# Kernel tuning notes

Measured on AMD Instinct MI355X. Metric: run time of the kernel, lower is better.

The kernel has to match this reference:

```python
import jax, jax.numpy as jnp
import numpy as np

NEG = 1e9  # mask value added to already-selected positions (original uses -1e9)


def setup_inputs() -> dict:
    key = jax.random.key(0)
    ks = jax.random.split(key, 12)
    B, N, M = 8, 2048, 256
    s = 0.05  # keep gates/softmax in a sane range
    return dict(
        node_embedding=jax.random.normal(ks[0], (B, N, M), dtype=jnp.float32),
        z_g=jax.random.normal(ks[1], (B, M), dtype=jnp.float32) * s,
        decoder_init=jax.random.normal(ks[2], (M,), dtype=jnp.float32) * s,
        hidden0=jax.random.normal(ks[3], (M,), dtype=jnp.float32) * s,
        w_ih=jax.random.normal(ks[4], (4 * M, M), dtype=jnp.float32) * s,
        w_hh=jax.random.normal(ks[5], (4 * M, M), dtype=jnp.float32) * s,
        b_ih=jax.random.normal(ks[6], (4 * M,), dtype=jnp.float32) * s,
        b_hh=jax.random.normal(ks[7], (4 * M,), dtype=jnp.float32) * s,
        Wq=jax.random.normal(ks[8], (M, M), dtype=jnp.float32) * s,
        bq=jax.random.normal(ks[9], (M,), dtype=jnp.float32) * s,
        Wk=jax.random.normal(ks[10], (M, M), dtype=jnp.float32) * s,
        bk=jax.random.normal(ks[11], (M,), dtype=jnp.float32) * s,
    )


def reference(node_embedding, z_g, decoder_init, hidden0,
              w_ih, w_hh, b_ih, b_hh, Wq, bq, Wk, bk):
    # Returns the per-step masked softmax attention distributions [B, N, N]
    # (row t = distribution over boxes at decode step t; argmax of each row
    #  is the predicted order, and selected indices are masked out).
    N = node_embedding.shape[1]
    # LSTM input is the constant decoder_init every step -> precompute its proj.
    x_proj = decoder_init @ w_ih.T + b_ih  # [4M]

    def decode_one(z_g_b, node_emb_b):
        keys = node_emb_b @ Wk.T + bk  # [N, M] (self.key(node_embedding))

        def step(carry, _):
            h, c, used = carry
            # torch LSTMCell: gates ordered (i, f, g, o)
            gates = x_proj + h @ w_hh.T + b_hh  # [4M]
            i_g, f_g, g_g, o_g = jnp.split(gates, 4)
            i_g = jax.nn.sigmoid(i_g)
            f_g = jax.nn.sigmoid(f_g)
            g_g = jnp.tanh(g_g)
            o_g = jax.nn.sigmoid(o_g)
            c = f_g * c + i_g * g_g
            h = o_g * jnp.tanh(c)
            q = h @ Wq.T + bq                    # [M]
            scores = keys @ q                    # [N]
            scores = jnp.where(used, scores - NEG, scores)  # mask selected
            probs = jax.nn.softmax(scores)       # [N]
            idx = jnp.argmax(probs)              # top-1 pointer selection
            used = used.at[idx].set(True)
            return (h, c, used), probs

        init = (hidden0, z_g_b, jnp.zeros((N,), dtype=bool))
        _, probs = jax.lax.scan(step, init, None, length=N)
        return probs  # [N, N]

    return jax.vmap(decode_one)(z_g, node_embedding)  # [B, N, N]
```

## Files before the change

### kernel.cpp

```cpp
#include <hip/hip_runtime.h>
#include <cstdint>
#include <cstddef>

#define NB 8
#define NN 2048
#define MM 256

typedef unsigned long long u64;

__device__ __forceinline__ unsigned mapf(float f) {
  unsigned u = __float_as_uint(f + 0.f);
  return ((int)u >= 0) ? (u ^ 0x80000000u) : ~u;
}
__device__ __forceinline__ u64 shflx_u64(u64 v, int m) {
  unsigned lo = (unsigned)__shfl_xor((int)(unsigned)v, m);
  unsigned hi = (unsigned)__shfl_xor((int)(v >> 32), m);
  return ((u64)hi << 32) | lo;
}

__global__ __launch_bounds__(1024) void lstm_kernel(
    const float* __restrict__ z_g, const float* __restrict__ dec,
    const float* __restrict__ h0, const float* __restrict__ w_ih,
    const float* __restrict__ w_hh, const float* __restrict__ b_ih,
    const float* __restrict__ b_hh, float* __restrict__ Hall,
    u64* __restrict__ Pbuf)
{
  const int b = blockIdx.x;
  const int q = blockIdx.y;
  const int tid = threadIdx.x;
  const int w = tid >> 6;
  const int lane = tid & 63;
  const int rr = lane >> 3;
  const int c8 = lane & 7;
  const int lr = 8 * w + rr;
  const int g = lr >> 5;
  const int m = lr & 31;
  const int grow = g * 256 + 32 * q + m;

  __shared__ __align__(16) float hbuf[256];
  __shared__ __align__(16) float act[128];

  float wreg[32];
  {
    const float* wr = w_hh + (size_t)grow * MM + 32 * c8;
    #pragma unroll
    for (int jj = 0; jj < 8; ++jj) {
      float4 v = *(const float4*)(wr + 4 * ((jj + c8) & 7));
      wreg[4 * jj + 0] = v.x; wreg[4 * jj + 1] = v.y;
      wreg[4 * jj + 2] = v.z; wreg[4 * jj + 3] = v.w;
    }
  }

  float xb;
  {
    const float* wr = w_ih + (size_t)grow * MM + 32 * c8;
    float p = 0.f;
    #pragma unroll
    for (int i = 0; i < 8; ++i) {
      float4 wv = *(const float4*)(wr + 4 * i);
      float4 dv = *(const float4*)(dec + 32 * c8 + 4 * i);
      p += wv.x * dv.x + wv.y * dv.y + wv.z * dv.z + wv.w * dv.w;
    }
    p += __shfl_xor(p, 1); p += __shfl_xor(p, 2); p += __shfl_xor(p, 4);
    xb = p + b_ih[grow] + b_hh[grow];
  }

  float c_my = 0.f;
  if (tid < 32) c_my = z_g[b * MM + 32 * q + tid];
  if (tid < 256) hbuf[tid] = h0[tid];

  u64* Pb = Pbuf + (size_t)b * 512;
  float* Hb = Hall + (size_t)b * NN * MM + 32 * q;

  for (int tt = 0; tt < NN; ++tt) {
    if (tt > 0 && w < 4) {
      const int widx = (w << 6) + lane;
      const u64* pa = Pb + ((tt & 1) << 8) + widx;
      u64 v = __hip_atomic_load(pa, __ATOMIC_RELAXED,
                                __HIP_MEMORY_SCOPE_AGENT);
      bool ok = ((unsigned)(v >> 32) == (unsigned)tt);
      while (!__all((int)ok)) {
        if (!ok) {
          v = __hip_atomic_load(pa, __ATOMIC_RELAXED,
                                __HIP_MEMORY_SCOPE_AGENT);
          ok = ((unsigned)(v >> 32) == (unsigned)tt);
        }
      }
      hbuf[widx] = __uint_as_float((unsigned)v);
    }
    __syncthreads();

    float a0 = 0.f, a1 = 0.f, a2 = 0.f, a3 = 0.f;
    const float4* h4 = (const float4*)hbuf;
    #pragma unroll
    for (int jj = 0; jj < 8; ++jj) {
      float4 hv = h4[8 * c8 + ((jj + c8) & 7)];
      a0 = fmaf(hv.x, wreg[4 * jj + 0], a0);
      a1 = fmaf(hv.y, wreg[4 * jj + 1], a1);
      a2 = fmaf(hv.z, wreg[4 * jj + 2], a2);
      a3 = fmaf(hv.w, wreg[4 * jj + 3], a3);
    }
    float s = (a0 + a1) + (a2 + a3);
    s += __shfl_xor(s, 1); s += __shfl_xor(s, 2); s += __shfl_xor(s, 4);
    const float gsum = s + xb;

    float a;
    if ((w >> 2) == 2) { const float e = __expf(-2.f * gsum); a = 2.f / (1.f + e) - 1.f; }
    else               { a = 1.f / (1.f + __expf(-gsum)); }
    if (c8 == 0) act[lr] = a;
    __syncthreads();

    if (tid < 32) {
      const float i_g = act[tid], f_g = act[32 + tid];
      const float g_g = act[64 + tid], o_g = act[96 + tid];
      c_my = f_g * c_my + i_g * g_g;
      const float e2 = __expf(-2.f * c_my);
      const float hn = o_g * (2.f / (1.f + e2) - 1.f);
      const u64 pk = ((u64)(unsigned)(tt + 1) << 32) | (u64)__float_as_uint(hn);
      __hip_atomic_store(Pb + (((tt + 1) & 1) << 8) + 32 * q + tid, pk,
                         __ATOMIC_RELAXED, __HIP_MEMORY_SCOPE_AGENT);
      Hb[(size_t)tt * MM + tid] = hn;
    }
  }
}

__global__ __launch_bounds__(256) void gemm128(
    const float* __restrict__ A, const float* __restrict__ B,
    float* __restrict__ C, const float* __restrict__ bias,
    int K, int Ncol, long sA, long sB, long sC)
{
  __shared__ __align__(16) float As[32][132];
  __shared__ __align__(16) float Bs[32][132];
  const int tid = threadIdx.x;
  const int tx = tid & 15;
  const int ty = tid >> 4;
  const int row0 = blockIdx.y * 128;
  const int col0 = blockIdx.x * 128;
  const float* Ab = A + (size_t)blockIdx.z * (size_t)sA;
  const float* Bb = B + (size_t)blockIdx.z * (size_t)sB;
  float* Cb = C + (size_t)blockIdx.z * (size_t)sC;

  float acc[8][8];
  #pragma unroll
  for (int i = 0; i < 8; ++i)
    #pragma unroll
    for (int jj = 0; jj < 8; ++jj) acc[i][jj] = 0.f;

  for (int k0 = 0; k0 < K; k0 += 32) {
    #pragma unroll
    for (int it = 0; it < 4; ++it) {
      const int idx = tid + it * 256;
      const int r = idx >> 3;
      const int c4 = (idx & 7) << 2;
      float4 va = *(const float4*)(Ab + (size_t)(row0 + r) * K + k0 + c4);
      float4 vb = *(const float4*)(Bb + (size_t)(col0 + r) * K + k0 + c4);
      As[c4 + 0][r] = va.x; As[c4 + 1][r] = va.y;
      As[c4 + 2][r] = va.z; As[c4 + 3][r] = va.w;
      Bs[c4 + 0][r] = vb.x; Bs[c4 + 1][r] = vb.y;
      Bs[c4 + 2][r] = vb.z; Bs[c4 + 3][r] = vb.w;
    }
    __syncthreads();
    #pragma unroll
    for (int kk = 0; kk < 32; ++kk) {
      float4 a0 = *(const float4*)&As[kk][ty * 4];
      float4 a1 = *(const float4*)&As[kk][64 + ty * 4];
      float4 b0 = *(const float4*)&Bs[kk][tx * 4];
      float4 b1 = *(const float4*)&Bs[kk][64 + tx * 4];
      const float av[8] = {a0.x, a0.y, a0.z, a0.w, a1.x, a1.y, a1.z, a1.w};
      const float bv[8] = {b0.x, b0.y, b0.z, b0.w, b1.x, b1.y, b1.z, b1.w};
      #pragma unroll
      for (int i = 0; i < 8; ++i)
        #pragma unroll
        for (int jj = 0; jj < 8; ++jj)
          acc[i][jj] = fmaf(av[i], bv[jj], acc[i][jj]);
    }
    __syncthreads();
  }

  #pragma unroll
  for (int i = 0; i < 8; ++i) {
    const int r = row0 + ((i < 4) ? (ty * 4 + i) : (64 + ty * 4 + i - 4));
    float* cp = Cb + (size_t)r * Ncol + col0;
    float4 o0, o1;
    float* o0p = &o0.x; float* o1p = &o1.x;
    #pragma unroll
    for (int jj = 0; jj < 4; ++jj) {
      float v0 = acc[i][jj], v1 = acc[i][jj + 4];
      if (bias) {
        v0 += bias[col0 + tx * 4 + jj];
        v1 += bias[col0 + 64 + tx * 4 + jj];
      }
      o0p[jj] = v0; o1p[jj] = v1;
    }
    *(float4*)(cp + tx * 4) = o0;
    *(float4*)(cp + 64 + tx * 4) = o1;
  }
}

__global__ __launch_bounds__(512) void select_block(
    const float* __restrict__ S, int* __restrict__ sel)
{
  const int b = blockIdx.x;
  const int tid = threadIdx.x;
  const int w = tid >> 6;
  const int lane = tid & 63;
  const float* Sb = S + (size_t)b * NN * NN + 4 * tid;
  int* selb = sel + b * NN;

  __shared__ u64 partial[2][8];

  for (int i = tid; i < NN; i += 512) selb[i] = 0x7fffffff;
  __syncthreads();

  unsigned mybits = 0;
  const unsigned base = 2047u - 4u * (unsigned)tid;

  auto stepf = [&](float4 v, int t) {
    u64 k0 = (mybits & 1u) ? 0 : (((u64)mapf(v.x) << 32) | (base - 0u));
    u64 k1 = (mybits & 2u) ? 0 : (((u64)mapf(v.y) << 32) | (base - 1u));
    u64 k2 = (mybits & 4u) ? 0 : (((u64)mapf(v.z) << 32) | (base - 2u));
    u64 k3 = (mybits & 8u) ? 0 : (((u64)mapf(v.w) << 32) | (base - 3u));
    u64 k = k0 > k1 ? k0 : k1;
    if (k2 > k) k = k2;
    if (k3 > k) k = k3;
    #pragma unroll
    for (int off = 1; off < 64; off <<= 1) {
      u64 o = shflx_u64(k, off);
      if (o > k) k = o;
    }
    if (lane == 0) partial[t & 1][w] = k;
    __syncthreads();
    u64 pk = partial[t & 1][lane & 7];
    #pragma unroll
    for (int off = 1; off < 8; off <<= 1) {
      u64 o = shflx_u64(pk, off);
      if (o > pk) pk = o;
    }
    const int idx = 2047 - (int)(pk & 0x7ff);
    if ((idx >> 2) == tid) mybits |= 1u << (idx & 3);
    if (tid == 0) selb[idx] = t;
  };

  float4 r0 = *(const float4*)(Sb + (size_t)0 * NN);
  float4 r1 = *(const float4*)(Sb + (size_t)1 * NN);
  float4 r2 = *(const float4*)(Sb + (size_t)2 * NN);
  float4 r3 = *(const float4*)(Sb + (size_t)3 * NN);
  for (int t = 0; t < NN; t += 4) {
    const size_t p4 = (size_t)((t + 4 < NN) ? t + 4 : NN - 1) * NN;
    const size_t p5 = (size_t)((t + 5 < NN) ? t + 5 : NN - 1) * NN;
    const size_t p6 = (size_t)((t + 6 < NN) ? t + 6 : NN - 1) * NN;
    const size_t p7 = (size_t)((t + 7 < NN) ? t + 7 : NN - 1) * NN;
    stepf(r0, t);     r0 = *(const float4*)(Sb + p4);
    stepf(r1, t + 1); r1 = *(const float4*)(Sb + p5);
    stepf(r2, t + 2); r2 = *(const float4*)(Sb + p6);
    stepf(r3, t + 3); r3 = *(const float4*)(Sb + p7);
  }
}

__global__ __launch_bounds__(256) void softmax_kernel(
    float* __restrict__ out, const int* __restrict__ sel)
{
  const int t = blockIdx.x;
  const int b = blockIdx.y;
  const int tid = threadIdx.x;
  float* row = out + ((size_t)b * NN + t) * NN;
  const int* selb = sel + b * NN;
  __shared__ float red[8];

  float v[8];
  int sl[8];
  #pragma unroll
  for (int u = 0; u < 2; ++u) {
    float4 f = *(const float4*)(row + u * 1024 + tid * 4);
    int4 s4 = *(const int4*)(selb + u * 1024 + tid * 4);
    v[u * 4 + 0] = f.x; v[u * 4 + 1] = f.y; v[u * 4 + 2] = f.z; v[u * 4 + 3] = f.w;
    sl[u * 4 + 0] = s4.x; sl[u * 4 + 1] = s4.y; sl[u * 4 + 2] = s4.z; sl[u * 4 + 3] = s4.w;
  }

  float mx = -3.0e38f;
  #pragma unroll
  for (int e = 0; e < 8; ++e)
    if (sl[e] >= t) mx = fmaxf(mx, v[e]);
  #pragma unroll
  for (int off = 1; off < 64; off <<= 1) mx = fmaxf(mx, __shfl_xor(mx, off));
  if ((tid & 63) == 0) red[tid >> 6] = mx;
  __syncthreads();
  mx = fmaxf(fmaxf(red[0], red[1]), fmaxf(red[2], red[3]));

  float e8[8];
  float sum = 0.f;
  #pragma unroll
  for (int e = 0; e < 8; ++e) {
    float ex = (sl[e] >= t) ? __expf(v[e] - mx) : 0.f;
    e8[e] = ex;
    sum += ex;
  }
  #pragma unroll
  for (int off = 1; off < 64; off <<= 1) sum += __shfl_xor(sum, off);
  if ((tid & 63) == 0) red[4 + (tid >> 6)] = sum;
  __syncthreads();
  sum = red[4] + red[5] + red[6] + red[7];
  const float inv = 1.f / sum;

  #pragma unroll
  for (int u = 0; u < 2; ++u) {
    float4 o;
    o.x = e8[u * 4 + 0] * inv; o.y = e8[u * 4 + 1] * inv;
    o.z = e8[u * 4 + 2] * inv; o.w = e8[u * 4 + 3] * inv;
    *(float4*)(row + u * 1024 + tid * 4) = o;
  }
}

extern "C" void kernel_launch(void* const* d_in, const int* in_sizes, int n_in,
                              void* d_out, int out_size, void* d_ws, size_t ws_size,
                              hipStream_t stream)
{
  (void)in_sizes; (void)n_in; (void)out_size; (void)ws_size;
  const float* emb  = (const float*)d_in[0];
  const float* z_g  = (const float*)d_in[1];
  const float* dec  = (const float*)d_in[2];
  const float* h0   = (const float*)d_in[3];
  const float* w_ih = (const float*)d_in[4];
  const float* w_hh = (const float*)d_in[5];
  const float* b_ih = (const float*)d_in[6];
  const float* b_hh = (const float*)d_in[7];
  const float* Wq   = (const float*)d_in[8];
  const float* bq   = (const float*)d_in[9];
  const float* Wk   = (const float*)d_in[10];
  const float* bk   = (const float*)d_in[11];
  float* out = (float*)d_out;
  float* ws  = (float*)d_ws;

  float* keys  = ws;
  float* Q     = ws + 4194304;
  u64*   Pbuf  = (u64*)(ws + 8388608);
  int*   sel   = (int*)(ws + 8396800);
  float* Hall  = out;

  hipMemsetAsync(Pbuf, 0, 4096 * sizeof(u64), stream);

  lstm_kernel<<<dim3(NB, 8), 1024, 0, stream>>>(
      z_g, dec, h0, w_ih, w_hh, b_ih, b_hh, Hall, Pbuf);

  gemm128<<<dim3(MM / 128, (NB * NN) / 128, 1), 256, 0, stream>>>(
      Hall, Wq, Q, bq, MM, MM, 0, 0, 0);

  gemm128<<<dim3(MM / 128, (NB * NN) / 128, 1), 256, 0, stream>>>(
      emb, Wk, keys, bk, MM, MM, 0, 0, 0);

  gemm128<<<dim3(NN / 128, NN / 128, NB), 256, 0, stream>>>(
      Q, keys, out, nullptr, MM, NN,
      (long)NN * MM, (long)NN * MM, (long)NN * NN);

  select_block<<<NB, 512, 0, stream>>>(out, sel);

  softmax_kernel<<<dim3(NN, NB), 256, 0, stream>>>(out, sel);
}
```

Measured before the change: 4.808 ms.

## Halve LSTM block size, keep gates per wave, drop second barrier

The LSTM recurrence kernel now runs 512 threads per block, and each thread computes two gate rows held in registers. The gate layout is arranged so that all four gates for a hidden unit sit in the same wavefront. Cell and hidden updates are therefore gathered with cross-lane shuffles instead of through shared memory. This removes one __syncthreads per step, and a double-buffered hbuf avoids a write-after-read race. The cost is more registers per thread, and the serial chain per step now runs two dot products in each thread.

```diff
diff --git a/kernel.cpp b/kernel.cpp
--- a/kernel.cpp
+++ b/kernel.cpp
@@ -18,7 +18,7 @@
   return ((u64)hi << 32) | lo;
 }
 
-__global__ __launch_bounds__(1024) void lstm_kernel(
+__global__ __launch_bounds__(512) void lstm_kernel(
     const float* __restrict__ z_g, const float* __restrict__ dec,
     const float* __restrict__ h0, const float* __restrict__ w_ih,
     const float* __restrict__ w_hh, const float* __restrict__ b_ih,
@@ -30,47 +30,59 @@
   const int tid = threadIdx.x;
   const int w = tid >> 6;
   const int lane = tid & 63;
-  const int rr = lane >> 3;
+  const int r8 = lane >> 3;
   const int c8 = lane & 7;
-  const int lr = 8 * w + rr;
-  const int g = lr >> 5;
-  const int m = lr & 31;
-  const int grow = g * 256 + 32 * q + m;
-
-  __shared__ __align__(16) float hbuf[256];
-  __shared__ __align__(16) float act[128];
-
-  float wreg[32];
+  const int g = r8 >> 1;
+  const int ml_lo = 4 * w + (r8 & 1);
+  const int grow_lo = g * 256 + 32 * q + ml_lo;
+  const int grow_hi = grow_lo + 2;
+  const int ml_own = r8 & 3;
+
+  __shared__ __align__(16) float hbuf[2][256];
+
+  float wlo[32], whi[32];
   {
-    const float* wr = w_hh + (size_t)grow * MM + 32 * c8;
+    const float* wr0 = w_hh + (size_t)grow_lo * MM + 32 * c8;
+    const float* wr1 = w_hh + (size_t)grow_hi * MM + 32 * c8;
     #pragma unroll
     for (int jj = 0; jj < 8; ++jj) {
-      float4 v = *(const float4*)(wr + 4 * ((jj + c8) & 7));
-      wreg[4 * jj + 0] = v.x; wreg[4 * jj + 1] = v.y;
-      wreg[4 * jj + 2] = v.z; wreg[4 * jj + 3] = v.w;
-    }
-  }
-
-  float xb;
+      const int sl = 4 * ((jj + c8) & 7);
+      float4 v = *(const float4*)(wr0 + sl);
+      wlo[4 * jj + 0] = v.x; wlo[4 * jj + 1] = v.y;
+      wlo[4 * jj + 2] = v.z; wlo[4 * jj + 3] = v.w;
+      float4 u = *(const float4*)(wr1 + sl);
+      whi[4 * jj + 0] = u.x; whi[4 * jj + 1] = u.y;
+      whi[4 * jj + 2] = u.z; whi[4 * jj + 3] = u.w;
+    }
+  }
+
+  float xb_lo, xb_hi;
   {
-    const float* wr = w_ih + (size_t)grow * MM + 32 * c8;
-    float p = 0.f;
+    const float* wr0 = w_ih + (size_t)grow_lo * MM + 32 * c8;
+    const float* wr1 = w_ih + (size_t)grow_hi * MM + 32 * c8;
+    float p0 = 0.f, p1 = 0.f;
     #pragma unroll
     for (int i = 0; i < 8; ++i) {
-      float4 wv = *(const float4*)(wr + 4 * i);
       float4 dv = *(const float4*)(dec + 32 * c8 + 4 * i);
-      p += wv.x * dv.x + wv.y * dv.y + wv.z * dv.z + wv.w * dv.w;
-    }
-    p += __shfl_xor(p, 1); p += __shfl_xor(p, 2); p += __shfl_xor(p, 4);
-    xb = p + b_ih[grow] + b_hh[grow];
-  }
-
-  float c_my = 0.f;
-  if (tid < 32) c_my = z_g[b * MM + 32 * q + tid];
-  if (tid < 256) hbuf[tid] = h0[tid];
+      float4 a = *(const float4*)(wr0 + 4 * i);
+      float4 c = *(const float4*)(wr1 + 4 * i);
+      p0 += a.x * dv.x + a.y * dv.y + a.z * dv.z + a.w * dv.w;
+      p1 += c.x * dv.x + c.y * dv.y + c.z * dv.z + c.w * dv.w;
+    }
+    p0 += __shfl_xor(p0, 1); p0 += __shfl_xor(p0, 2); p0 += __shfl_xor(p0, 4);
+    p1 += __shfl_xor(p1, 1); p1 += __shfl_xor(p1, 2); p1 += __shfl_xor(p1, 4);
+    xb_lo = p0 + b_ih[grow_lo] + b_hh[grow_lo];
+    xb_hi = p1 + b_ih[grow_hi] + b_hh[grow_hi];
+  }
+
+  float c_my = z_g[b * MM + 32 * q + 4 * w + ml_own];
+  if (tid < 256) hbuf[0][tid] = h0[tid];
 
   u64* Pb = Pbuf + (size_t)b * 512;
-  float* Hb = Hall + (size_t)b * NN * MM + 32 * q;
+  float* Hb = Hall + (size_t)b * NN * MM;
+
+  const bool istanh = (g == 2);
+  const float kmul = istanh ? -2.f : -1.f;
 
   for (int tt = 0; tt < NN; ++tt) {
     if (tt > 0 && w < 4) {
@@ -86,40 +98,63 @@
           ok = ((unsigned)(v >> 32) == (unsigned)tt);
         }
       }
-      hbuf[widx] = __uint_as_float((unsigned)v);
+      hbuf[tt & 1][widx] = __uint_as_float((unsigned)v);
     }
     __syncthreads();
 
-    float a0 = 0.f, a1 = 0.f, a2 = 0.f, a3 = 0.f;
-    const float4* h4 = (const float4*)hbuf;
+    const float4* h4 = (const float4*)hbuf[tt & 1];
+    float l0 = 0.f, l1 = 0.f, l2 = 0.f, l3 = 0.f;
+    float m0 = 0.f, m1 = 0.f, m2 = 0.f, m3 = 0.f;
     #pragma unroll
     for (int jj = 0; jj < 8; ++jj) {
       float4 hv = h4[8 * c8 + ((jj + c8) & 7)];
-      a0 = fmaf(hv.x, wreg[4 * jj + 0], a0);
-      a1 = fmaf(hv.y, wreg[4 * jj + 1], a1);
-      a2 = fmaf(hv.z, wreg[4 * jj + 2], a2);
-      a3 = fmaf(hv.w, wreg[4 * jj + 3], a3);
-    }
-    float s = (a0 + a1) + (a2 + a3);
-    s += __shfl_xor(s, 1); s += __shfl_xor(s, 2); s += __shfl_xor(s, 4);
-    const float gsum = s + xb;
-
-    float a;
-    if ((w >> 2) == 2) { const float e = __expf(-2.f * gsum); a = 2.f / (1.f + e) - 1.f; }
-    else               { a = 1.f / (1.f + __expf(-gsum)); }
-    if (c8 == 0) act[lr] = a;
-    __syncthreads();
-
-    if (tid < 32) {
-      const float i_g = act[tid], f_g = act[32 + tid];
-      const float g_g = act[64 + tid], o_g = act[96 + tid];
-      c_my = f_g * c_my + i_g * g_g;
-      const float e2 = __expf(-2.f * c_my);
-      const float hn = o_g * (2.f / (1.f + e2) - 1.f);
+      l0 = fmaf(hv.x, wlo[4 * jj + 0], l0);
+      l1 = fmaf(hv.y, wlo[4 * jj + 1], l1);
+      l2 = fmaf(hv.z, wlo[4 * jj + 2], l2);
+      l3 = fmaf(hv.w, wlo[4 * jj + 3], l3);
+      m0 = fmaf(hv.x, whi[4 * jj + 0], m0);
+      m1 = fmaf(hv.y, whi[4 * jj + 1], m1);
+      m2 = fmaf(hv.z, whi[4 * jj + 2], m2);
+      m3 = fmaf(hv.w, whi[4 * jj + 3], m3);
+    }
+    float s_lo = (l0 + l1) + (l2 + l3);
+    float s_hi = (m0 + m1) + (m2 + m3);
+    s_lo += __shfl_xor(s_lo, 1); s_lo += __shfl_xor(s_lo, 2); s_lo += __shfl_xor(s_lo, 4);
+    s_hi += __shfl_xor(s_hi, 1); s_hi += __shfl_xor(s_hi, 2); s_hi += __shfl_xor(s_hi, 4);
+    const float g_lo = s_lo + xb_lo;
+    const float g_hi = s_hi + xb_hi;
+
+    float e = __expf(kmul * g_lo);
+    float sg = 1.f / (1.f + e);
+    const float a_lo = istanh ? 2.f * sg - 1.f : sg;
+    e = __expf(kmul * g_hi);
+    sg = 1.f / (1.f + e);
+    const float a_hi = istanh ? 2.f * sg - 1.f : sg;
+
+    const int baseLane = 8 * (r8 & 1) + c8;
+    const bool lohalf = (r8 & 2) == 0;
+    float gi, gf, gg_, go;
+    {
+      float tl = __shfl(a_lo, baseLane);      float th = __shfl(a_hi, baseLane);
+      gi = lohalf ? tl : th;
+      tl = __shfl(a_lo, baseLane + 16);       th = __shfl(a_hi, baseLane + 16);
+      gf = lohalf ? tl : th;
+      tl = __shfl(a_lo, baseLane + 32);       th = __shfl(a_hi, baseLane + 32);
+      gg_ = lohalf ? tl : th;
+      tl = __shfl(a_lo, baseLane + 48);       th = __shfl(a_hi, baseLane + 48);
+      go = lohalf ? tl : th;
+    }
+
+    c_my = gf * c_my + gi * gg_;
+    const float e2 = __expf(-2.f * c_my);
+    const float hn = go * (2.f / (1.f + e2) - 1.f);
+
+    if (c8 == 0 && r8 < 4) {
+      const int mi = 32 * q + 4 * w + r8;
       const u64 pk = ((u64)(unsigned)(tt + 1) << 32) | (u64)__float_as_uint(hn);
-      __hip_atomic_store(Pb + (((tt + 1) & 1) << 8) + 32 * q + tid, pk,
+      __hip_atomic_store(Pb + (((tt + 1) & 1) << 8) + mi, pk,
                          __ATOMIC_RELAXED, __HIP_MEMORY_SCOPE_AGENT);
-      Hb[(size_t)tt * MM + tid] = hn;
+      Hb[(size_t)tt * MM + mi] = hn;
     }
   }
 }
@@ -339,7 +374,7 @@
 
   hipMemsetAsync(Pbuf, 0, 4096 * sizeof(u64), stream);
 
-  lstm_kernel<<<dim3(NB, 8), 1024, 0, stream>>>(
+  lstm_kernel<<<dim3(NB, 8), 512, 0, stream>>>(
       z_g, dec, h0, w_ih, w_hh, b_ih, b_hh, Hall, Pbuf);
 
   gemm128<<<dim3(MM / 128, (NB * NN) / 128, 1), 256, 0, stream>>>(
```

Result: slower. 6.637 ms (+38.0%).

## Remap LSTM gate rows per wave to drop second barrier and use shuffles

Applied to the files above, without the earlier changes.

Reassigns hidden units so each wave holds all four gate rows (i,f,g,o) for two hidden units. The gate activations can then be combined with wave shuffles instead of a shared-memory act buffer and a second __syncthreads per step. The h buffer is double-buffered so the single barrier per step is enough, and the spin-wait on the cross-block h exchange keeps three outstanding loads in flight to cut polling latency. The cost is extra polling traffic and redundant cell-state updates across lanes.

```diff
diff --git a/kernel.cpp b/kernel.cpp
--- a/kernel.cpp
+++ b/kernel.cpp
@@ -16,6 +16,9 @@
   unsigned lo = (unsigned)__shfl_xor((int)(unsigned)v, m);
   unsigned hi = (unsigned)__shfl_xor((int)(v >> 32), m);
   return ((u64)hi << 32) | lo;
+}
+__device__ __forceinline__ u64 agent_load(const u64* p) {
+  return __hip_atomic_load(p, __ATOMIC_RELAXED, __HIP_MEMORY_SCOPE_AGENT);
 }
 
 __global__ __launch_bounds__(1024) void lstm_kernel(
@@ -30,15 +33,14 @@
   const int tid = threadIdx.x;
   const int w = tid >> 6;
   const int lane = tid & 63;
-  const int rr = lane >> 3;
+  const int r8 = lane >> 3;
   const int c8 = lane & 7;
-  const int lr = 8 * w + rr;
-  const int g = lr >> 5;
-  const int m = lr & 31;
-  const int grow = g * 256 + 32 * q + m;
-
-  __shared__ __align__(16) float hbuf[256];
-  __shared__ __align__(16) float act[128];
+  const int g = r8 >> 1;
+  const int p = r8 & 1;
+  const int ml = 2 * w + p;
+  const int grow = g * 256 + 32 * q + ml;
+
+  __shared__ __align__(16) float hbuf[2][256];
 
   float wreg[32];
   {
@@ -54,44 +56,49 @@
   float xb;
   {
     const float* wr = w_ih + (size_t)grow * MM + 32 * c8;
-    float p = 0.f;
+    float pcc = 0.f;
     #pragma unroll
     for (int i = 0; i < 8; ++i) {
       float4 wv = *(const float4*)(wr + 4 * i);
       float4 dv = *(const float4*)(dec + 32 * c8 + 4 * i);
-      p += wv.x * dv.x + wv.y * dv.y + wv.z * dv.z + wv.w * dv.w;
-    }
-    p += __shfl_xor(p, 1); p += __shfl_xor(p, 2); p += __shfl_xor(p, 4);
-    xb = p + b_ih[grow] + b_hh[grow];
-  }
-
-  float c_my = 0.f;
-  if (tid < 32) c_my = z_g[b * MM + 32 * q + tid];
-  if (tid < 256) hbuf[tid] = h0[tid];
+      pcc += wv.x * dv.x + wv.y * dv.y + wv.z * dv.z + wv.w * dv.w;
+    }
+    pcc += __shfl_xor(pcc, 1); pcc += __shfl_xor(pcc, 2); pcc += __shfl_xor(pcc, 4);
+    xb = pcc + b_ih[grow] + b_hh[grow];
+  }
+
+  float c_my = z_g[b * MM + 32 * q + ml];
+  if (tid < 256) hbuf[0][tid] = h0[tid];
 
   u64* Pb = Pbuf + (size_t)b * 512;
-  float* Hb = Hall + (size_t)b * NN * MM + 32 * q;
+  float* Hb = Hall + (size_t)b * NN * MM;
+
+  const bool istanh = (g == 2);
+  const float kmul = istanh ? -2.f : -1.f;
 
   for (int tt = 0; tt < NN; ++tt) {
     if (tt > 0 && w < 4) {
       const int widx = (w << 6) + lane;
       const u64* pa = Pb + ((tt & 1) << 8) + widx;
-      u64 v = __hip_atomic_load(pa, __ATOMIC_RELAXED,
-                                __HIP_MEMORY_SCOPE_AGENT);
-      bool ok = ((unsigned)(v >> 32) == (unsigned)tt);
-      while (!__all((int)ok)) {
-        if (!ok) {
-          v = __hip_atomic_load(pa, __ATOMIC_RELAXED,
-                                __HIP_MEMORY_SCOPE_AGENT);
-          ok = ((unsigned)(v >> 32) == (unsigned)tt);
-        }
+      const unsigned tg = (unsigned)tt;
+      u64 v0 = agent_load(pa);
+      u64 v1 = agent_load(pa);
+      u64 v2 = agent_load(pa);
+      u64 v;
+      for (;;) {
+        if (__all((int)((unsigned)(v0 >> 32) == tg))) { v = v0; break; }
+        v0 = agent_load(pa);
+        if (__all((int)((unsigned)(v1 >> 32) == tg))) { v = v1; break; }
+        v1 = agent_load(pa);
+        if (__all((int)((unsigned)(v2 >> 32) == tg))) { v = v2; break; }
+        v2 = agent_load(pa);
       }
-      hbuf[widx] = __uint_as_float((unsigned)v);
+      hbuf[tt & 1][widx] = __uint_as_float((unsigned)v);
     }
     __syncthreads();
 
+    const float4* h4 = (const float4*)hbuf[tt & 1];
     float a0 = 0.f, a1 = 0.f, a2 = 0.f, a3 = 0.f;
-    const float4* h4 = (const float4*)hbuf;
     #pragma unroll
     for (int jj = 0; jj < 8; ++jj) {
       float4 hv = h4[8 * c8 + ((jj + c8) & 7)];
@@ -104,22 +111,26 @@
     s += __shfl_xor(s, 1); s += __shfl_xor(s, 2); s += __shfl_xor(s, 4);
     const float gsum = s + xb;
 
-    float a;
-    if ((w >> 2) == 2) { const float e = __expf(-2.f * gsum); a = 2.f / (1.f + e) - 1.f; }
-    else               { a = 1.f / (1.f + __expf(-gsum)); }
-    if (c8 == 0) act[lr] = a;
-    __syncthreads();
-
-    if (tid < 32) {
-      const float i_g = act[tid], f_g = act[32 + tid];
-      const float g_g = act[64 + tid], o_g = act[96 + tid];
-      c_my = f_g * c_my + i_g * g_g;
-      const float e2 = __expf(-2.f * c_my);
-      const float hn = o_g * (2.f / (1.f + e2) - 1.f);
+    const float e = __expf(kmul * gsum);
+    const float sg = 1.f / (1.f + e);
+    const float a = istanh ? 2.f * sg - 1.f : sg;
+
+    const int bl = 8 * p + c8;
+    const float gi  = __shfl(a, bl);
+    const float gf  = __shfl(a, 16 + bl);
+    const float gg_ = __shfl(a, 32 + bl);
+    const float go  = __shfl(a, 48 + bl);
+
+    c_my = gf * c_my + gi * gg_;
+    const float e2 = __expf(-2.f * c_my);
+    const float hn = go * (2.f / (1.f + e2) - 1.f);
+
+    if (r8 < 2 && c8 == 0) {
+      const int mi = 32 * q + ml;
       const u64 pk = ((u64)(unsigned)(tt + 1) << 32) | (u64)__float_as_uint(hn);
-      __hip_atomic_store(Pb + (((tt + 1) & 1) << 8) + 32 * q + tid, pk,
+      __hip_atomic_store(Pb + (((tt + 1) & 1) << 8) + mi, pk,
                          __ATOMIC_RELAXED, __HIP_MEMORY_SCOPE_AGENT);
-      Hb[(size_t)tt * MM + tid] = hn;
+      Hb[(size_t)tt * MM + mi] = hn;
     }
   }
 }
```

Measured after the change: 9.289 ms. 93.2% more time.
